# Kernel tuning notes

Hardware: AMD Instinct MI355X
Metric: run time of the kernel (lower is better)

The kernel has to match this reference:

```python
import jax, jax.numpy as jnp
import numpy as np

N_BINS = 64
INPUT_DIM = 8
R = 1.2
BOUND = 10.0
BETA = 1e-06
N = 2097152


def _mesh_and_elmt():
    m = N_BINS / 2
    idx = jnp.arange(N_BINS + 1, dtype=jnp.float32) - m
    x1L = BOUND * (R - 1.0) / (R ** m - 1.0)
    xr = (1.0 - R ** jnp.abs(idx)) / (1.0 - R)
    xr = jnp.where(idx >= 0, x1L * xr, -x1L * xr)
    xr = (xr + BOUND) / (2.0 * BOUND)
    mesh = jnp.concatenate([jnp.zeros((1,), jnp.float32), xr[1:-1], jnp.ones((1,), jnp.float32)])  # [n_bins+1]
    elmt = mesh[1:] - mesh[:-1]  # [n_bins]
    return mesh, elmt


def _pdf_normalize(p, elmt):
    # pdf: [n_bins+1, d]; F_ref: [n_bins, d] cumulative bin integrals
    p0 = jnp.full((1, INPUT_DIM), BETA, jnp.float32)
    ep = jnp.exp(p)
    px = ep * ((elmt[:-1] + elmt[1:]) / 2.0)[:, None]
    scale = (1.0 - (elmt[0] + elmt[-1]) * BETA / 2.0) / jnp.sum(px, 0, keepdims=True)
    px = scale * ep
    pdf = jnp.concatenate([p0, px, p0], 0)
    cell = (pdf[:-1] + pdf[1:]) / 2.0 * elmt[:, None]  # [n_bins, d]
    F_ref = jnp.concatenate([jnp.zeros((1, INPUT_DIM), jnp.float32),
                             jnp.cumsum(cell, 0)[:N_BINS - 1]], 0)
    return pdf, F_ref


def setup_inputs() -> dict:
    key = jax.random.key(0)
    k1, k2 = jax.random.split(key)
    x = jax.random.normal(k1, (N, INPUT_DIM), dtype=jnp.float32)
    logdet = jnp.zeros((N, 1), dtype=jnp.float32)
    p = jax.random.normal(k2, (N_BINS - 1, INPUT_DIM), dtype=jnp.float32)
    return {"x": x, "logdet": logdet, "p": p}


def reference(x, logdet, p):
    mesh, elmt = _mesh_and_elmt()
    pdf, F_ref = _pdf_normalize(p, elmt)

    xs = (x + BOUND) / (2.0 * BOUND)  # [N, d] in [0,1] for covered points
    k = jnp.searchsorted(mesh, xs, side='right') - 1  # [N, d]
    cover = (k >= 0) & (k <= N_BINS - 1)
    k = jnp.clip(k, 0, N_BINS - 1)
    col = jnp.arange(INPUT_DIM)[None, :]

    v1 = pdf[k, col]            # [N, d]
    v2 = pdf[k + 1, col]
    xm = xs - mesh[k]
    h = elmt[k]
    F_pre = F_ref[k, col]

    y = jnp.where(cover, F_pre + xm * xm / 2.0 * (v2 - v1) / h + xm * v1, xs)
    dld = jnp.where(cover, xm * (v2 - v1) / h + v1, 1.0)
    logdet = logdet + jnp.sum(jnp.log(dld), -1, keepdims=True)

    y = y * 2.0 * BOUND - BOUND
    y = jnp.where(y > BOUND, BETA * (y - BOUND) + BOUND, y)
    logdet = logdet + jnp.sum(jnp.log(jnp.where(y > BOUND, BETA, 1.0)), -1, keepdims=True)
    y = jnp.where(y < -BOUND, BETA * (y + BOUND) - BOUND, y)
    logdet = logdet + jnp.sum(jnp.log(jnp.where(y < -BOUND, BETA, 1.0)), -1, keepdims=True)
    return y, logdet
```

## Files before the change

kernel.cpp:

```cpp
#include <hip/hip_runtime.h>
#include <hip/hip_bf16.h>
#include <math.h>

#define NDIM   8
#define NBINS  64
#define LOG_BETA   (-13.815510557964274f)
#define LN2F       0.69314718055994531f
#define ALPHA      34.0821892f
#define INV_LOG2R  3.80178401692393f

__global__ __launch_bounds__(256) void cdfq_fused(const float* __restrict__ x,
                                                  const float* __restrict__ logdet_in,
                                                  const float* __restrict__ p,
                                                  float* __restrict__ y_out,
                                                  float* __restrict__ ld_out,
                                                  int n)
{
    __shared__ float  mesh[65];
    __shared__ float  elmt[64];
    __shared__ float  sc[NDIM];
    __shared__ float  pdfs[NDIM][65];
    __shared__ float  cell[NDIM][64];
    __shared__ float4 stbl[NDIM * NBINS];

    const int t = threadIdx.x;

    if (t < 65) {
        float fidx = (float)t - 32.0f;
        float a = fabsf(fidx);
        float x1L = 2.0f / (powf(1.2f, 32.0f) - 1.0f);
        float xr = x1L * (powf(1.2f, a) - 1.0f) / 0.2f;
        xr = (fidx >= 0.0f) ? xr : -xr;
        xr = (xr + 10.0f) / 20.0f;
        if (t == 0)  xr = 0.0f;
        if (t == 64) xr = 1.0f;
        mesh[t] = xr;
    }
    for (int idx = t; idx < 63 * NDIM; idx += 256) {
        int d = idx & 7, k = idx >> 3;
        pdfs[d][k + 1] = expf(p[k * NDIM + d]);
    }
    if (t < NDIM) { pdfs[t][0] = 1e-6f; pdfs[t][64] = 1e-6f; }
    __syncthreads();
    if (t < 64) elmt[t] = mesh[t + 1] - mesh[t];
    __syncthreads();

    if (t < 64) {
        for (int d = 0; d < NDIM; ++d) {
            float w = 0.0f;
            if (t < 63) w = pdfs[d][t + 1] * 0.5f * (elmt[t] + elmt[t + 1]);
            for (int off = 32; off > 0; off >>= 1) w += __shfl_down(w, off);
            if (t == 0) sc[d] = (1.0f - (elmt[0] + elmt[63]) * 5e-7f) / w;
        }
    }
    __syncthreads();
    for (int idx = t; idx < 63 * NDIM; idx += 256) {
        int d = idx & 7, k = idx >> 3;
        pdfs[d][k + 1] *= sc[d];
    }
    __syncthreads();
    for (int idx = t; idx < NDIM * NBINS; idx += 256) {
        int d = idx >> 6, k = idx & 63;
        cell[d][k] = 0.5f * (pdfs[d][k] + pdfs[d][k + 1]) * elmt[k];
    }
    __syncthreads();
    if (t < 64) {
        for (int d = 0; d < NDIM; ++d) {
            float c0 = cell[d][t];
            float v = c0;
            for (int off = 1; off < 64; off <<= 1) {
                float w = __shfl_up(v, off);
                if (t >= off) v += w;
            }
            float Fpre = v - c0;
            float v1 = pdfs[d][t];
            float v2 = pdfs[d][t + 1];
            stbl[d * 64 + t] = make_float4(v1, (v2 - v1) / elmt[t], Fpre, mesh[t]);
        }
    }
    __syncthreads();

    const int stride = gridDim.x * blockDim.x;
    for (int i = blockIdx.x * blockDim.x + t; i < n; i += stride) {
        const float4* xv = (const float4*)x + 2 * (size_t)i;
        float4 xa = xv[0];
        float4 xb = xv[1];
        float ld = logdet_in[i];

        float xd[8] = {xa.x, xa.y, xa.z, xa.w, xb.x, xb.y, xb.z, xb.w};
        float yd[8], dd[8];

#pragma unroll
        for (int d = 0; d < 8; ++d) {
            float xo = xd[d];
            float xs = fmaf(xo, 0.05f, 0.5f);
            float u  = fabsf(xo);
            float g  = __log2f(fmaf(ALPHA, u, 1.0f)) * INV_LOG2R;
            int jp = (int)fminf(g, 31.0f);
            int jn = (int)ceilf(fminf(g, 32.0f));
            int k  = (xo >= 0.0f) ? (32 + jp) : (32 - jn);

            float4 tb = stbl[(d << 6) + k];
            float xm  = xs - tb.w;
            bool cov  = (xs >= 0.0f) && (xs < 1.0f);

            float yc = tb.z + xm * fmaf(0.5f * xm, tb.y, tb.x);
            float dl = fmaf(xm, tb.y, tb.x);
            float yy = cov ? yc : xs;
            dd[d]    = cov ? dl : 1.0f;

            yy = fmaf(yy, 20.0f, -10.0f);
            if (yy > 10.0f)  { yy = fmaf(1e-6f, yy - 10.0f, 10.0f);  ld += LOG_BETA; }
            if (yy < -10.0f) { yy = fmaf(1e-6f, yy + 10.0f, -10.0f); ld += LOG_BETA; }
            yd[d] = yy;
        }

        float l01 = __log2f(dd[0] * dd[1]);
        float l23 = __log2f(dd[2] * dd[3]);
        float l45 = __log2f(dd[4] * dd[5]);
        float l67 = __log2f(dd[6] * dd[7]);
        ld = fmaf((l01 + l23) + (l45 + l67), LN2F, ld);

        float4* yo = (float4*)y_out + 2 * (size_t)i;
        yo[0] = make_float4(yd[0], yd[1], yd[2], yd[3]);
        yo[1] = make_float4(yd[4], yd[5], yd[6], yd[7]);
        ld_out[i] = ld;
    }
}

extern "C" void kernel_launch(void* const* d_in, const int* in_sizes, int n_in,
                              void* d_out, int out_size, void* d_ws, size_t ws_size,
                              hipStream_t stream) {
    const float* x      = (const float*)d_in[0];
    const float* logdet = (const float*)d_in[1];
    const float* p      = (const float*)d_in[2];

    const int n = in_sizes[1];
    float* y_out  = (float*)d_out;
    float* ld_out = (float*)d_out + (size_t)n * NDIM;

    const int block = 256;
    const int grid  = 2048;
    cdfq_fused<<<grid, block, 0, stream>>>(x, logdet, p, y_out, ld_out, n);
}
```

Measured before the change: 140.1 us.

## Batch four rows per thread with upfront loads and size grid to cover input

```diff
diff --git a/kernel.cpp b/kernel.cpp
--- a/kernel.cpp
+++ b/kernel.cpp
@@ -9,12 +9,12 @@
 #define ALPHA      34.0821892f
 #define INV_LOG2R  3.80178401692393f
 
-__global__ __launch_bounds__(256) void cdfq_fused(const float* __restrict__ x,
-                                                  const float* __restrict__ logdet_in,
-                                                  const float* __restrict__ p,
-                                                  float* __restrict__ y_out,
-                                                  float* __restrict__ ld_out,
-                                                  int n)
+__global__ __launch_bounds__(256, 8) void cdfq_fused(const float* __restrict__ x,
+                                                     const float* __restrict__ logdet_in,
+                                                     const float* __restrict__ p,
+                                                     float* __restrict__ y_out,
+                                                     float* __restrict__ ld_out,
+                                                     int n)
 {
     __shared__ float  mesh[65];
     __shared__ float  elmt[64];
@@ -80,14 +80,30 @@
     }
     __syncthreads();
 
-    const int stride = gridDim.x * blockDim.x;
-    for (int i = blockIdx.x * blockDim.x + t; i < n; i += stride) {
-        const float4* xv = (const float4*)x + 2 * (size_t)i;
-        float4 xa = xv[0];
-        float4 xb = xv[1];
-        float ld = logdet_in[i];
+    const int T  = gridDim.x * blockDim.x;
+    const int i0 = blockIdx.x * blockDim.x + t;
+    const float4* xv = (const float4*)x;
 
-        float xd[8] = {xa.x, xa.y, xa.z, xa.w, xb.x, xb.y, xb.z, xb.w};
+    int   ii[4];
+    float4 A[4], B[4];
+    float  L[4];
+#pragma unroll
+    for (int j = 0; j < 4; ++j) {
+        int i = i0 + j * T;
+        ii[j] = i;
+        if (i < n) {
+            A[j] = xv[2 * (size_t)i];
+            B[j] = xv[2 * (size_t)i + 1];
+            L[j] = logdet_in[i];
+        }
+    }
+
+#pragma unroll
+    for (int j = 0; j < 4; ++j) {
+        int i = ii[j];
+        if (i >= n) continue;
+        float ld = L[j];
+        float xd[8] = {A[j].x, A[j].y, A[j].z, A[j].w, B[j].x, B[j].y, B[j].z, B[j].w};
         float yd[8], dd[8];
 
 #pragma unroll
@@ -140,6 +156,6 @@
     float* ld_out = (float*)d_out + (size_t)n * NDIM;
 
     const int block = 256;
-    const int grid  = 2048;
+    const int grid  = (n + block * 4 - 1) / (block * 4);
     cdfq_fused<<<grid, block, 0, stream>>>(x, logdet, p, y_out, ld_out, n);
 }
```

After: 150.6 us. 1.08x slower.

## Prefetch first inputs before table build and software-pipeline the grid-stride loop

Applied to the files above, without the earlier changes.

```diff
diff --git a/kernel.cpp b/kernel.cpp
--- a/kernel.cpp
+++ b/kernel.cpp
@@ -9,21 +9,32 @@
 #define ALPHA      34.0821892f
 #define INV_LOG2R  3.80178401692393f
 
-__global__ __launch_bounds__(256) void cdfq_fused(const float* __restrict__ x,
-                                                  const float* __restrict__ logdet_in,
-                                                  const float* __restrict__ p,
-                                                  float* __restrict__ y_out,
-                                                  float* __restrict__ ld_out,
-                                                  int n)
+__global__ __launch_bounds__(256, 8) void cdfq_fused(const float* __restrict__ x,
+                                                     const float* __restrict__ logdet_in,
+                                                     const float* __restrict__ p,
+                                                     float* __restrict__ y_out,
+                                                     float* __restrict__ ld_out,
+                                                     int n)
 {
     __shared__ float  mesh[65];
     __shared__ float  elmt[64];
     __shared__ float  sc[NDIM];
     __shared__ float  pdfs[NDIM][65];
-    __shared__ float  cell[NDIM][64];
     __shared__ float4 stbl[NDIM * NBINS];
 
-    const int t = threadIdx.x;
+    const int t  = threadIdx.x;
+    const int T  = gridDim.x * blockDim.x;
+    const int i0 = blockIdx.x * blockDim.x + t;
+    const int iters = n / T;
+    const float4* xv = (const float4*)x;
+
+    float4 Ac, Bc; float Lc;
+    if (iters > 0) {
+        Ac = xv[2 * (size_t)i0];
+        Bc = xv[2 * (size_t)i0 + 1];
+        Lc = logdet_in[i0];
+    }
+    __builtin_amdgcn_sched_barrier(0);
 
     if (t < 65) {
         float fidx = (float)t - 32.0f;
@@ -59,14 +70,9 @@
         pdfs[d][k + 1] *= sc[d];
     }
     __syncthreads();
-    for (int idx = t; idx < NDIM * NBINS; idx += 256) {
-        int d = idx >> 6, k = idx & 63;
-        cell[d][k] = 0.5f * (pdfs[d][k] + pdfs[d][k + 1]) * elmt[k];
-    }
-    __syncthreads();
     if (t < 64) {
         for (int d = 0; d < NDIM; ++d) {
-            float c0 = cell[d][t];
+            float c0 = 0.5f * (pdfs[d][t] + pdfs[d][t + 1]) * elmt[t];
             float v = c0;
             for (int off = 1; off < 64; off <<= 1) {
                 float w = __shfl_up(v, off);
@@ -80,14 +86,9 @@
     }
     __syncthreads();
 
-    const int stride = gridDim.x * blockDim.x;
-    for (int i = blockIdx.x * blockDim.x + t; i < n; i += stride) {
-        const float4* xv = (const float4*)x + 2 * (size_t)i;
-        float4 xa = xv[0];
-        float4 xb = xv[1];
-        float ld = logdet_in[i];
-
-        float xd[8] = {xa.x, xa.y, xa.z, xa.w, xb.x, xb.y, xb.z, xb.w};
+    auto body = [&](float4 A, float4 B, float Lin, int i) {
+        float ld = Lin;
+        float xd[8] = {A.x, A.y, A.z, A.w, B.x, B.y, B.z, B.w};
         float yd[8], dd[8];
 
 #pragma unroll
@@ -125,6 +126,30 @@
         yo[0] = make_float4(yd[0], yd[1], yd[2], yd[3]);
         yo[1] = make_float4(yd[4], yd[5], yd[6], yd[7]);
         ld_out[i] = ld;
+    };
+
+    for (int j = 0; j < iters; ++j) {
+        float4 An, Bn; float Ln;
+        const bool more = (j + 1 < iters);
+        if (more) {
+            size_t ix = (size_t)i0 + (size_t)(j + 1) * T;
+            An = xv[2 * ix];
+            Bn = xv[2 * ix + 1];
+            Ln = logdet_in[ix];
+        }
+        __builtin_amdgcn_sched_barrier(0);
+
+        body(Ac, Bc, Lc, i0 + j * T);
+
+        if (more) { Ac = An; Bc = Bn; Lc = Ln; }
+    }
+
+    int ir = i0 + iters * T;
+    if (ir < n) {
+        float4 A = xv[2 * (size_t)ir];
+        float4 B = xv[2 * (size_t)ir + 1];
+        float  L = logdet_in[ir];
+        body(A, B, L, ir);
     }
 }
 
@@ -140,6 +165,7 @@
     float* ld_out = (float*)d_out + (size_t)n * NDIM;
 
     const int block = 256;
-    const int grid  = 2048;
+    int grid = 2048;
+    if (grid * block > n) grid = (n + block - 1) / block;
     cdfq_fused<<<grid, block, 0, stream>>>(x, logdet, p, y_out, ld_out, n);
 }
```

Result: no change. 139.6 us (-0.3%).
